# Kernel optimization log

Hardware: AMD Instinct MI355X
Metric: run time of the kernel (lower is better)

Reference implementation:

```python
import jax, jax.numpy as jnp
import numpy as np

E, B, L, H1, H2, C = 8, 4096, 512, 1024, 512, 40


def setup_inputs() -> dict:
    key = jax.random.key(0)
    ks = jax.random.split(key, 9)
    return {
        "x_s": jax.random.normal(ks[0], (B, L), jnp.float32),
        "x_p": jax.random.normal(ks[1], (B, L), jnp.float32),
        "W1": jax.random.normal(ks[2], (E, 2 * L, H1), jnp.float32) / np.sqrt(2 * L).astype(np.float32),
        "b1": jax.random.normal(ks[3], (E, H1), jnp.float32) * 0.01,
        "W2": jax.random.normal(ks[4], (E, H1, H2), jnp.float32) / np.sqrt(H1).astype(np.float32),
        "b2": jax.random.normal(ks[5], (E, H2), jnp.float32) * 0.01,
        "W3": jax.random.normal(ks[6], (E, H2, C), jnp.float32) / np.sqrt(H2).astype(np.float32),
        "b3": jax.random.normal(ks[7], (E, C), jnp.float32) * 0.01,
        "sub_module_label": jax.random.randint(ks[8], (B,), 0, E, dtype=jnp.int32),
        "sub_id": 0,
    }


def reference(x_s, x_p, W1, b1, W2, b2, W3, b3, sub_module_label, sub_id):
    # Encoders (EEGNet/SCN/DCN) abstracted as identity: x_s / x_p are latent features.
    # Cls_HEAD.forward: x = cat([x_p, x_s], dim=1); per-sample routed 3-layer ELU MLP head.
    # Dropout is identity in eval mode.
    x = jnp.concatenate([x_p, x_s], axis=1)                      # [B, 2L]
    h = jax.nn.elu(jnp.einsum('bi,eih->ebh', x, W1) + b1[:, None, :])   # [E, B, H1]
    h = jax.nn.elu(jnp.einsum('ebh,ehk->ebk', h, W2) + b2[:, None, :])  # [E, B, H2]
    out_all = jnp.einsum('ebk,ekc->ebc', h, W3) + b3[:, None, :]        # [E, B, C]
    # select each sample's routed expert output
    bidx = jnp.arange(x.shape[0])
    return out_all[sub_module_label, bidx]                       # [B, C]
```

## Files before the change

kernel.cpp:

```cpp
#include <hip/hip_runtime.h>
#include <hip/hip_bf16.h>
#include <math.h>

#define En   8
#define Bn   4096
#define Ln   512
#define K1n  1024
#define H1n  1024
#define H2n  512
#define Cn   40
#define NP3  48

typedef unsigned short u16;
typedef __attribute__((ext_vector_type(8))) short bf16x8;
typedef __attribute__((ext_vector_type(4))) float f32x4;

__device__ __forceinline__ u16 f2b(float f) {
    union { float f; unsigned int u; } v; v.f = f;
    unsigned int r = v.u + 0x7FFF + ((v.u >> 16) & 1);
    return (u16)(r >> 16);
}

__device__ __forceinline__ void g2l16(const void* g, void* l) {
    __builtin_amdgcn_global_load_lds(
        (const __attribute__((address_space(1))) unsigned int*)(unsigned long long)g,
        (__attribute__((address_space(3))) unsigned int*)(unsigned int)(unsigned long long)l,
        16, 0, 0);
}

#define PB_X0   1
#define PB_X    256
#define PB_W1   2048
#define PB_W2   1024
#define PB_W3   128
#define PB_TOT  (PB_X0 + PB_X + PB_W1 + PB_W2 + PB_W3)

__device__ __forceinline__ void wtrans64(
    const float* __restrict__ Wsrc, u16* __restrict__ Wdst,
    int K, int N, int k0, int n0, int tid, float* sm )
{
    #pragma unroll
    for (int s = 0; s < 4; s++) {
        int idx = tid + s * 256;
        int kk = idx >> 4, c4 = (idx & 15) * 4;
        float4 v = *(const float4*)&Wsrc[(size_t)(k0 + kk) * N + n0 + c4];
        float* row = sm + kk * 65 + c4;
        row[0] = v.x; row[1] = v.y; row[2] = v.z; row[3] = v.w;
    }
    __syncthreads();
    #pragma unroll
    for (int s = 0; s < 4; s++) {
        int idx = tid + s * 256;
        int nn = idx >> 4, kc = (idx & 15) * 4;
        ushort4 o = make_ushort4(f2b(sm[(kc + 0) * 65 + nn]), f2b(sm[(kc + 1) * 65 + nn]),
                                 f2b(sm[(kc + 2) * 65 + nn]), f2b(sm[(kc + 3) * 65 + nn]));
        *(ushort4*)&Wdst[(size_t)(n0 + nn) * K + k0 + kc] = o;
    }
}

__global__ __launch_bounds__(256) void prep_kernel(
    const float* __restrict__ xs, const float* __restrict__ xp,
    const float* __restrict__ W1, const float* __restrict__ W2,
    const float* __restrict__ W3, const int* __restrict__ label,
    int* __restrict__ meta, int* __restrict__ perm,
    u16* __restrict__ Xb, u16* __restrict__ W1t,
    u16* __restrict__ W2t, u16* __restrict__ W3t)
{
    __shared__ __align__(16) float sm[64 * 65];
    const int bid = blockIdx.x;
    const int tid = threadIdx.x;

    if (bid == 0) {
        int* cnt = (int*)sm;
        int* off = cnt + En;
        if (tid < En) cnt[tid] = 0;
        __syncthreads();
        for (int b = tid; b < Bn; b += 256) atomicAdd(&cnt[label[b]], 1);
        __syncthreads();
        if (tid == 0) {
            int run = 0;
            for (int e = 0; e < En; e++) { off[e] = run; run += cnt[e]; }
            off[En] = run;
        }
        __syncthreads();
        if (tid < En) cnt[tid] = off[tid];
        __syncthreads();
        for (int b = tid; b < Bn; b += 256) {
            int e = label[b];
            perm[atomicAdd(&cnt[e], 1)] = b;
        }
        if (tid <= En) meta[tid] = off[tid];
    } else if (bid < PB_X0 + PB_X) {
        int r0 = (bid - PB_X0) * 16;
        #pragma unroll 4
        for (int s = 0; s < 16; s++) {
            int r = r0 + s;
            int k = tid * 4;
            const float* src = (k < Ln) ? (xp + (size_t)r * Ln + k)
                                        : (xs + (size_t)r * Ln + (k - Ln));
            float4 v = *(const float4*)src;
            *(ushort4*)&Xb[(size_t)r * K1n + k] =
                make_ushort4(f2b(v.x), f2b(v.y), f2b(v.z), f2b(v.w));
        }
    } else if (bid < PB_X0 + PB_X + PB_W1) {
        int b = bid - (PB_X0 + PB_X);
        int e = b >> 8, rem = b & 255;
        int k0 = (rem >> 4) * 64, n0 = (rem & 15) * 64;
        wtrans64(W1 + (size_t)e * K1n * H1n, W1t + (size_t)e * H1n * K1n,
                 K1n, H1n, k0, n0, tid, sm);
    } else if (bid < PB_X0 + PB_X + PB_W1 + PB_W2) {
        int b = bid - (PB_X0 + PB_X + PB_W1);
        int e = b >> 7, rem = b & 127;
        int k0 = (rem >> 3) * 64, n0 = (rem & 7) * 64;
        wtrans64(W2 + (size_t)e * H1n * H2n, W2t + (size_t)e * H2n * H1n,
                 H1n, H2n, k0, n0, tid, sm);
    } else {
        int b = bid - (PB_X0 + PB_X + PB_W1 + PB_W2);
        int e = b >> 4, k0 = (b & 15) * 32;
        const float* src = W3 + (size_t)e * H2n * Cn;
        u16* dst = W3t + (size_t)e * NP3 * H2n;
        float* t = sm;
        #pragma unroll
        for (int s = 0; s < 5; s++) {
            int idx = tid + s * 256;
            int kk = idx / Cn, nn = idx - kk * Cn;
            if (kk < 32) t[kk * 41 + nn] = src[(size_t)(k0 + kk) * Cn + nn];
        }
        __syncthreads();
        #pragma unroll
        for (int s = 0; s < 6; s++) {
            int idx = tid + s * 256;
            int nn = idx >> 5, kk = idx & 31;
            float v = (nn < Cn) ? t[kk * 41 + nn] : 0.f;
            dst[(size_t)nn * H2n + k0 + kk] = f2b(v);
        }
    }
}

template <int K, int N, bool GATHER>
__global__ __launch_bounds__(256) void mfma_gemm(
    const u16* __restrict__ A, const u16* __restrict__ Wt,
    const float* __restrict__ bias, const int* __restrict__ meta,
    const int* __restrict__ perm, u16* __restrict__ out)
{
    constexpr int TM = 128, TN = 128, BK = 32;
    __shared__ __align__(16) u16 As[TM * BK];
    __shared__ __align__(16) u16 Bs[TN * BK];
    __shared__ int s_off[En + 1];

    const int tid = threadIdx.x;
    if (tid <= En) s_off[tid] = meta[tid];
    __syncthreads();

    int expert = -1, row0 = 0, acc_t = 0;
    const int bx = blockIdx.x;
    for (int e = 0; e < En; e++) {
        int c = s_off[e + 1] - s_off[e];
        int t = (c + TM - 1) / TM;
        if (expert < 0 && bx < acc_t + t) {
            expert = e;
            row0 = s_off[e] + (bx - acc_t) * TM;
        }
        acc_t += t;
    }
    if (expert < 0) return;
    const int rowmax = s_off[expert + 1] - 1;

    const int col0 = blockIdx.y * TN;
    const u16* Wexp = Wt + (size_t)expert * N * K;

    const int lane = tid & 63;
    const int wid = tid >> 6;
    const int wm = (wid & 1) * 64;
    const int wn = (wid >> 1) * 64;
    const int l15 = lane & 15;
    const int lq = lane >> 4;

    const u16* aptr[2];
    const u16* bptr[2];
    u16* alds[2]; u16* blds[2];
    #pragma unroll
    for (int s = 0; s < 2; s++) {
        int idx = tid + s * 256;
        int rl = idx >> 2, c = idx & 3;
        int kq = c ^ (rl & 3);
        int rg = row0 + rl; if (rg > rowmax) rg = rowmax;
        if (GATHER) rg = perm[rg];
        aptr[s] = A + (size_t)rg * K + kq * 8;
        bptr[s] = Wexp + (size_t)(col0 + rl) * K + kq * 8;
        alds[s] = &As[idx * 8];
        blds[s] = &Bs[idx * 8];
    }

    const int rsw = l15 & 3;

    f32x4 acc[4][4];
    #pragma unroll
    for (int i = 0; i < 4; i++)
        #pragma unroll
        for (int j = 0; j < 4; j++) acc[i][j] = (f32x4){0.f, 0.f, 0.f, 0.f};

    for (int k0 = 0; k0 < K; k0 += BK) {
        #pragma unroll
        for (int s = 0; s < 2; s++) {
            g2l16(aptr[s] + k0, alds[s]);
            g2l16(bptr[s] + k0, blds[s]);
        }
        __syncthreads();

        const int ksw = (lq ^ rsw) * 8;
        bf16x8 af[4], bf[4];
        #pragma unroll
        for (int i = 0; i < 4; i++)
            af[i] = *(const bf16x8*)&As[(wm + i * 16 + l15) * BK + ksw];
        #pragma unroll
        for (int j = 0; j < 4; j++)
            bf[j] = *(const bf16x8*)&Bs[(wn + j * 16 + l15) * BK + ksw];

        #pragma unroll
        for (int i = 0; i < 4; i++)
            #pragma unroll
            for (int j = 0; j < 4; j++)
                acc[i][j] = __builtin_amdgcn_mfma_f32_16x16x32_bf16(
                    af[i], bf[j], acc[i][j], 0, 0, 0);
        __syncthreads();
    }

    #pragma unroll
    for (int i = 0; i < 4; i++) {
        #pragma unroll
        for (int j = 0; j < 4; j++) {
            int col = col0 + wn + j * 16 + l15;
            float bv = bias[expert * N + col];
            #pragma unroll
            for (int r = 0; r < 4; r++) {
                int grow = row0 + wm + i * 16 + lq * 4 + r;
                if (grow <= rowmax) {
                    float v = acc[i][j][r] + bv;
                    v = (v > 0.f) ? v : (expf(v) - 1.f);
                    out[(size_t)grow * N + col] = f2b(v);
                }
            }
        }
    }
}

__global__ __launch_bounds__(256) void gemm3_mfma(
    const u16* __restrict__ h2, const u16* __restrict__ Wt3,
    const float* __restrict__ b3, const int* __restrict__ meta,
    const int* __restrict__ perm, float* __restrict__ out)
{
    constexpr int TM = 64, BK = 32;
    __shared__ __align__(16) u16 As[TM * BK];
    __shared__ __align__(16) u16 Bs[NP3 * BK];
    __shared__ int s_off[En + 1];

    const int tid = threadIdx.x;
    if (tid <= En) s_off[tid] = meta[tid];
    __syncthreads();

    int expert = -1, row0 = 0, acc_t = 0;
    const int bx = blockIdx.x;
    for (int e = 0; e < En; e++) {
        int c = s_off[e + 1] - s_off[e];
        int t = (c + TM - 1) / TM;
        if (expert < 0 && bx < acc_t + t) {
            expert = e;
            row0 = s_off[e] + (bx - acc_t) * TM;
        }
        acc_t += t;
    }
    if (expert < 0) return;
    const int rowmax = s_off[expert + 1] - 1;

    const int lane = tid & 63;
    const int wid = tid >> 6;
    const int l15 = lane & 15;
    const int lq = lane >> 4;

    const int rl = tid >> 2, c = tid & 3;
    const int kq = c ^ (rl & 3);
    int rg = row0 + rl; if (rg > rowmax) rg = rowmax;
    const u16* ag = h2 + (size_t)rg * H2n + kq * 8;
    const u16* bg = Wt3 + (size_t)expert * NP3 * H2n + (size_t)rl * H2n + kq * 8;
    u16* al = &As[tid * 8];
    u16* bl = &Bs[tid * 8];

    f32x4 acc[3];
    #pragma unroll
    for (int j = 0; j < 3; j++) acc[j] = (f32x4){0.f, 0.f, 0.f, 0.f};

    for (int k0 = 0; k0 < H2n; k0 += BK) {
        g2l16(ag + k0, al);
        if (tid < NP3 * 4) g2l16(bg + k0, bl);
        __syncthreads();

        const int ksw = (lq ^ (l15 & 3)) * 8;
        bf16x8 af = *(const bf16x8*)&As[(wid * 16 + l15) * BK + ksw];
        bf16x8 bf[3];
        #pragma unroll
        for (int j = 0; j < 3; j++)
            bf[j] = *(const bf16x8*)&Bs[(j * 16 + l15) * BK + ksw];
        #pragma unroll
        for (int j = 0; j < 3; j++)
            acc[j] = __builtin_amdgcn_mfma_f32_16x16x32_bf16(af, bf[j], acc[j], 0, 0, 0);
        __syncthreads();
    }

    #pragma unroll
    for (int j = 0; j < 3; j++) {
        int col = j * 16 + l15;
        if (col < Cn) {
            float bv = b3[expert * Cn + col];
            #pragma unroll
            for (int r = 0; r < 4; r++) {
                int grow = row0 + wid * 16 + lq * 4 + r;
                if (grow <= rowmax) {
                    int smp = perm[grow];
                    out[(size_t)smp * Cn + col] = acc[j][r] + bv;
                }
            }
        }
    }
}

extern "C" void kernel_launch(void* const* d_in, const int* in_sizes, int n_in,
                              void* d_out, int out_size, void* d_ws, size_t ws_size,
                              hipStream_t stream)
{
    const float* xs = (const float*)d_in[0];
    const float* xp = (const float*)d_in[1];
    const float* W1 = (const float*)d_in[2];
    const float* b1 = (const float*)d_in[3];
    const float* W2 = (const float*)d_in[4];
    const float* b2 = (const float*)d_in[5];
    const float* W3 = (const float*)d_in[6];
    const float* b3 = (const float*)d_in[7];
    const int* label = (const int*)d_in[8];
    float* out = (float*)d_out;

    char* ws = (char*)d_ws;
    int* meta = (int*)ws;
    int* perm = (int*)(ws + 64);
    u16* Xb  = (u16*)(ws + (64 << 10));
    u16* h2b = Xb;
    u16* W1t = (u16*)(ws + (64 << 10) + (8  << 20));
    u16* W2t = (u16*)(ws + (64 << 10) + (24 << 20));
    u16* h1b = (u16*)(ws + (64 << 10) + (32 << 20));
    u16* W3t = (u16*)(ws + (64 << 10) + (40 << 20));

    prep_kernel<<<PB_TOT, 256, 0, stream>>>(
        xs, xp, W1, W2, W3, label, meta, perm, Xb, W1t, W2t, W3t);

    mfma_gemm<K1n, H1n, true><<<dim3(40, H1n / 128), 256, 0, stream>>>(
        Xb, W1t, b1, meta, perm, h1b);
    mfma_gemm<H1n, H2n, false><<<dim3(40, H2n / 128), 256, 0, stream>>>(
        h1b, W2t, b2, meta, perm, h2b);

    gemm3_mfma<<<72, 256, 0, stream>>>(h2b, W3t, b3, meta, perm, out);
}
```

Measured before the change: 192.8 us.

## Fuse layer-3 GEMM into layer-2 epilogue and double-buffer GEMM K-loop

The third GEMM is folded into the layer-2 kernel epilogue. Each block stages its ELU'd h2 tile in LDS, multiplies it by the matching 128-column slice of W3, and atomically adds partial logits into the output, which the prep kernel pre-initialises with the per-sample b3 bias. The main GEMM loop also moves to BK=64 with double-buffered LDS prefetch and an 8-way XOR swizzle, to overlap global loads with MFMA work. This removes one launch and the h2 round-trip through memory, at the cost of float atomics (ordering changes rounding) and more LDS per block.

```diff
diff --git a/kernel.cpp b/kernel.cpp
--- a/kernel.cpp
+++ b/kernel.cpp
@@ -33,7 +33,8 @@
 #define PB_W1   2048
 #define PB_W2   1024
 #define PB_W3   128
-#define PB_TOT  (PB_X0 + PB_X + PB_W1 + PB_W2 + PB_W3)
+#define PB_OUT  64
+#define PB_TOT  (PB_X0 + PB_X + PB_W1 + PB_W2 + PB_W3 + PB_OUT)
 
 __device__ __forceinline__ void wtrans64(
     const float* __restrict__ Wsrc, u16* __restrict__ Wdst,
@@ -61,10 +62,12 @@
 __global__ __launch_bounds__(256) void prep_kernel(
     const float* __restrict__ xs, const float* __restrict__ xp,
     const float* __restrict__ W1, const float* __restrict__ W2,
-    const float* __restrict__ W3, const int* __restrict__ label,
+    const float* __restrict__ W3, const float* __restrict__ b3,
+    const int* __restrict__ label,
     int* __restrict__ meta, int* __restrict__ perm,
     u16* __restrict__ Xb, u16* __restrict__ W1t,
-    u16* __restrict__ W2t, u16* __restrict__ W3t)
+    u16* __restrict__ W2t, u16* __restrict__ W3t,
+    float* __restrict__ out)
 {
     __shared__ __align__(16) float sm[64 * 65];
     const int bid = blockIdx.x;
@@ -114,7 +117,7 @@
         int k0 = (rem >> 3) * 64, n0 = (rem & 7) * 64;
         wtrans64(W2 + (size_t)e * H1n * H2n, W2t + (size_t)e * H2n * H1n,
                  H1n, H2n, k0, n0, tid, sm);
-    } else {
+    } else if (bid < PB_X0 + PB_X + PB_W1 + PB_W2 + PB_W3) {
         int b = bid - (PB_X0 + PB_X + PB_W1 + PB_W2);
         int e = b >> 4, k0 = (b & 15) * 32;
         const float* src = W3 + (size_t)e * H2n * Cn;
@@ -134,37 +137,46 @@
             float v = (nn < Cn) ? t[kk * 41 + nn] : 0.f;
             dst[(size_t)nn * H2n + k0 + kk] = f2b(v);
         }
-    }
-}
-
-template <int K, int N, bool GATHER>
+    } else {
+        int b = bid - (PB_X0 + PB_X + PB_W1 + PB_W2 + PB_W3);
+        int r0 = b * 64;
+        #pragma unroll
+        for (int s = 0; s < 10; s++) {
+            int idx = tid + s * 256;
+            int r = r0 + idx / Cn;
+            int c = idx - (idx / Cn) * Cn;
+            out[(size_t)r * Cn + c] = b3[label[r] * Cn + c];
+        }
+    }
+}
+
+template <int K, int N, bool GATHER, bool FUSE3>
 __global__ __launch_bounds__(256) void mfma_gemm(
     const u16* __restrict__ A, const u16* __restrict__ Wt,
     const float* __restrict__ bias, const int* __restrict__ meta,
-    const int* __restrict__ perm, u16* __restrict__ out)
+    const int* __restrict__ perm, u16* __restrict__ outb,
+    const u16* __restrict__ Wt3, float* __restrict__ outf)
 {
-    constexpr int TM = 128, TN = 128, BK = 32;
-    __shared__ __align__(16) u16 As[TM * BK];
-    __shared__ __align__(16) u16 Bs[TN * BK];
-    __shared__ int s_off[En + 1];
+    constexpr int TM = 128, TN = 128, BK = 64;
+    constexpr int T = K / BK;
+    __shared__ __align__(16) u16 SM[32768];
 
     const int tid = threadIdx.x;
-    if (tid <= En) s_off[tid] = meta[tid];
-    __syncthreads();
-
-    int expert = -1, row0 = 0, acc_t = 0;
     const int bx = blockIdx.x;
+
+    int expert = -1, row0 = 0, rowmax = 0, acc_t = 0;
+    int prev = meta[0];
+    #pragma unroll
     for (int e = 0; e < En; e++) {
-        int c = s_off[e + 1] - s_off[e];
+        int nxt = meta[e + 1];
+        int c = nxt - prev;
         int t = (c + TM - 1) / TM;
         if (expert < 0 && bx < acc_t + t) {
-            expert = e;
-            row0 = s_off[e] + (bx - acc_t) * TM;
-        }
-        acc_t += t;
+            expert = e; row0 = prev + (bx - acc_t) * TM; rowmax = nxt - 1;
+        }
+        acc_t += t; prev = nxt;
     }
     if (expert < 0) return;
-    const int rowmax = s_off[expert + 1] - 1;
 
     const int col0 = blockIdx.y * TN;
     const u16* Wexp = Wt + (size_t)expert * N * K;
@@ -176,23 +188,21 @@
     const int l15 = lane & 15;
     const int lq = lane >> 4;
 
-    const u16* aptr[2];
-    const u16* bptr[2];
-    u16* alds[2]; u16* blds[2];
-    #pragma unroll
-    for (int s = 0; s < 2; s++) {
+    const u16* aptr[4]; const u16* bptr[4];
+    int aoff[4], boff[4];
+    #pragma unroll
+    for (int s = 0; s < 4; s++) {
         int idx = tid + s * 256;
-        int rl = idx >> 2, c = idx & 3;
-        int kq = c ^ (rl & 3);
+        int rl = idx >> 3, c = idx & 7;
+        int kq = c ^ (rl & 7);
         int rg = row0 + rl; if (rg > rowmax) rg = rowmax;
         if (GATHER) rg = perm[rg];
         aptr[s] = A + (size_t)rg * K + kq * 8;
         bptr[s] = Wexp + (size_t)(col0 + rl) * K + kq * 8;
-        alds[s] = &As[idx * 8];
-        blds[s] = &Bs[idx * 8];
-    }
-
-    const int rsw = l15 & 3;
+        aoff[s] = idx * 8;
+        boff[s] = 8192 + idx * 8;
+    }
+    const int csw = l15 & 7;
 
     f32x4 acc[4][4];
     #pragma unroll
@@ -200,124 +210,118 @@
         #pragma unroll
         for (int j = 0; j < 4; j++) acc[i][j] = (f32x4){0.f, 0.f, 0.f, 0.f};
 
-    for (int k0 = 0; k0 < K; k0 += BK) {
-        #pragma unroll
-        for (int s = 0; s < 2; s++) {
-            g2l16(aptr[s] + k0, alds[s]);
-            g2l16(bptr[s] + k0, blds[s]);
-        }
-        __syncthreads();
-
-        const int ksw = (lq ^ rsw) * 8;
-        bf16x8 af[4], bf[4];
-        #pragma unroll
-        for (int i = 0; i < 4; i++)
-            af[i] = *(const bf16x8*)&As[(wm + i * 16 + l15) * BK + ksw];
-        #pragma unroll
-        for (int j = 0; j < 4; j++)
-            bf[j] = *(const bf16x8*)&Bs[(wn + j * 16 + l15) * BK + ksw];
-
-        #pragma unroll
-        for (int i = 0; i < 4; i++)
+    #pragma unroll
+    for (int s = 0; s < 4; s++) {
+        g2l16(aptr[s], &SM[aoff[s]]);
+        g2l16(bptr[s], &SM[boff[s]]);
+    }
+
+    for (int t = 0; t < T; t++) {
+        __syncthreads();
+        const u16* As = &SM[(t & 1) * 16384];
+        const u16* Bs = As + 8192;
+        if (t + 1 < T) {
+            int base = ((t + 1) & 1) * 16384;
+            int ko = (t + 1) * BK;
+            #pragma unroll
+            for (int s = 0; s < 4; s++) {
+                g2l16(aptr[s] + ko, &SM[base + aoff[s]]);
+                g2l16(bptr[s] + ko, &SM[base + boff[s]]);
+            }
+        }
+        bf16x8 af[4][2], bf[4][2];
+        #pragma unroll
+        for (int h = 0; h < 2; h++) {
+            const int ksw = (((h * 4 + lq) ^ csw)) * 8;
+            #pragma unroll
+            for (int i = 0; i < 4; i++)
+                af[i][h] = *(const bf16x8*)&As[(wm + i * 16 + l15) * BK + ksw];
             #pragma unroll
             for (int j = 0; j < 4; j++)
-                acc[i][j] = __builtin_amdgcn_mfma_f32_16x16x32_bf16(
-                    af[i], bf[j], acc[i][j], 0, 0, 0);
-        __syncthreads();
-    }
-
-    #pragma unroll
-    for (int i = 0; i < 4; i++) {
-        #pragma unroll
-        for (int j = 0; j < 4; j++) {
-            int col = col0 + wn + j * 16 + l15;
-            float bv = bias[expert * N + col];
-            #pragma unroll
-            for (int r = 0; r < 4; r++) {
-                int grow = row0 + wm + i * 16 + lq * 4 + r;
-                if (grow <= rowmax) {
+                bf[j][h] = *(const bf16x8*)&Bs[(wn + j * 16 + l15) * BK + ksw];
+        }
+        #pragma unroll
+        for (int h = 0; h < 2; h++)
+            #pragma unroll
+            for (int i = 0; i < 4; i++)
+                #pragma unroll
+                for (int j = 0; j < 4; j++)
+                    acc[i][j] = __builtin_amdgcn_mfma_f32_16x16x32_bf16(
+                        af[i][h], bf[j][h], acc[i][j], 0, 0, 0);
+    }
+
+    if (!FUSE3) {
+        #pragma unroll
+        for (int i = 0; i < 4; i++) {
+            #pragma unroll
+            for (int j = 0; j < 4; j++) {
+                int col = col0 + wn + j * 16 + l15;
+                float bv = bias[expert * N + col];
+                #pragma unroll
+                for (int r = 0; r < 4; r++) {
+                    int grow = row0 + wm + i * 16 + lq * 4 + r;
+                    if (grow <= rowmax) {
+                        float v = acc[i][j][r] + bv;
+                        v = (v > 0.f) ? v : (expf(v) - 1.f);
+                        outb[(size_t)grow * N + col] = f2b(v);
+                    }
+                }
+            }
+        }
+    } else {
+        __syncthreads();
+        u16* H = &SM[0];
+        #pragma unroll
+        for (int i = 0; i < 4; i++) {
+            #pragma unroll
+            for (int j = 0; j < 4; j++) {
+                int col = wn + j * 16 + l15;
+                float bv = bias[expert * N + col0 + col];
+                #pragma unroll
+                for (int r = 0; r < 4; r++) {
                     float v = acc[i][j][r] + bv;
                     v = (v > 0.f) ? v : (expf(v) - 1.f);
-                    out[(size_t)grow * N + col] = f2b(v);
+                    H[(wm + i * 16 + lq * 4 + r) * 136 + col] = f2b(v);
                 }
             }
         }
-    }
-}
-
-__global__ __launch_bounds__(256) void gemm3_mfma(
-    const u16* __restrict__ h2, const u16* __restrict__ Wt3,
-    const float* __restrict__ b3, const int* __restrict__ meta,
-    const int* __restrict__ perm, float* __restrict__ out)
-{
-    constexpr int TM = 64, BK = 32;
-    __shared__ __align__(16) u16 As[TM * BK];
-    __shared__ __align__(16) u16 Bs[NP3 * BK];
-    __shared__ int s_off[En + 1];
-
-    const int tid = threadIdx.x;
-    if (tid <= En) s_off[tid] = meta[tid];
-    __syncthreads();
-
-    int expert = -1, row0 = 0, acc_t = 0;
-    const int bx = blockIdx.x;
-    for (int e = 0; e < En; e++) {
-        int c = s_off[e + 1] - s_off[e];
-        int t = (c + TM - 1) / TM;
-        if (expert < 0 && bx < acc_t + t) {
-            expert = e;
-            row0 = s_off[e] + (bx - acc_t) * TM;
-        }
-        acc_t += t;
-    }
-    if (expert < 0) return;
-    const int rowmax = s_off[expert + 1] - 1;
-
-    const int lane = tid & 63;
-    const int wid = tid >> 6;
-    const int l15 = lane & 15;
-    const int lq = lane >> 4;
-
-    const int rl = tid >> 2, c = tid & 3;
-    const int kq = c ^ (rl & 3);
-    int rg = row0 + rl; if (rg > rowmax) rg = rowmax;
-    const u16* ag = h2 + (size_t)rg * H2n + kq * 8;
-    const u16* bg = Wt3 + (size_t)expert * NP3 * H2n + (size_t)rl * H2n + kq * 8;
-    u16* al = &As[tid * 8];
-    u16* bl = &Bs[tid * 8];
-
-    f32x4 acc[3];
-    #pragma unroll
-    for (int j = 0; j < 3; j++) acc[j] = (f32x4){0.f, 0.f, 0.f, 0.f};
-
-    for (int k0 = 0; k0 < H2n; k0 += BK) {
-        g2l16(ag + k0, al);
-        if (tid < NP3 * 4) g2l16(bg + k0, bl);
-        __syncthreads();
-
-        const int ksw = (lq ^ (l15 & 3)) * 8;
-        bf16x8 af = *(const bf16x8*)&As[(wid * 16 + l15) * BK + ksw];
-        bf16x8 bf[3];
-        #pragma unroll
-        for (int j = 0; j < 3; j++)
-            bf[j] = *(const bf16x8*)&Bs[(j * 16 + l15) * BK + ksw];
-        #pragma unroll
-        for (int j = 0; j < 3; j++)
-            acc[j] = __builtin_amdgcn_mfma_f32_16x16x32_bf16(af, bf[j], acc[j], 0, 0, 0);
-        __syncthreads();
-    }
-
-    #pragma unroll
-    for (int j = 0; j < 3; j++) {
-        int col = j * 16 + l15;
-        if (col < Cn) {
-            float bv = b3[expert * Cn + col];
-            #pragma unroll
-            for (int r = 0; r < 4; r++) {
-                int grow = row0 + wid * 16 + lq * 4 + r;
-                if (grow <= rowmax) {
-                    int smp = perm[grow];
-                    out[(size_t)smp * Cn + col] = acc[j][r] + bv;
+        __syncthreads();
+        const int rh = (wid & 1) * 64;
+        const int kb = (wid >> 1) * 64;
+        f32x4 a3[4][3];
+        #pragma unroll
+        for (int i = 0; i < 4; i++)
+            #pragma unroll
+            for (int j = 0; j < 3; j++) a3[i][j] = (f32x4){0.f, 0.f, 0.f, 0.f};
+        #pragma unroll
+        for (int ki = 0; ki < 2; ki++) {
+            int kl = kb + ki * 32;
+            bf16x8 ha[4];
+            #pragma unroll
+            for (int i = 0; i < 4; i++)
+                ha[i] = *(const bf16x8*)&H[(rh + i * 16 + l15) * 136 + kl + lq * 8];
+            #pragma unroll
+            for (int j = 0; j < 3; j++) {
+                bf16x8 wb = *(const bf16x8*)
+                    &Wt3[((size_t)expert * NP3 + j * 16 + l15) * H2n + col0 + kl + lq * 8];
+                #pragma unroll
+                for (int i = 0; i < 4; i++)
+                    a3[i][j] = __builtin_amdgcn_mfma_f32_16x16x32_bf16(
+                        ha[i], wb, a3[i][j], 0, 0, 0);
+            }
+        }
+        #pragma unroll
+        for (int j = 0; j < 3; j++) {
+            int col = j * 16 + l15;
+            if (col < Cn) {
+                #pragma unroll
+                for (int i = 0; i < 4; i++) {
+                    #pragma unroll
+                    for (int r = 0; r < 4; r++) {
+                        int grow = row0 + rh + i * 16 + lq * 4 + r;
+                        if (grow <= rowmax)
+                            atomicAdd(&outf[(size_t)perm[grow] * Cn + col], a3[i][j][r]);
+                    }
                 }
             }
         }
@@ -343,19 +347,17 @@
     int* meta = (int*)ws;
     int* perm = (int*)(ws + 64);
     u16* Xb  = (u16*)(ws + (64 << 10));
-    u16* h2b = Xb;
     u16* W1t = (u16*)(ws + (64 << 10) + (8  << 20));
     u16* W2t = (u16*)(ws + (64 << 10) + (24 << 20));
     u16* h1b = (u16*)(ws + (64 << 10) + (32 << 20));
     u16* W3t = (u16*)(ws + (64 << 10) + (40 << 20));
 
     prep_kernel<<<PB_TOT, 256, 0, stream>>>(
-        xs, xp, W1, W2, W3, label, meta, perm, Xb, W1t, W2t, W3t);
-
-    mfma_gemm<K1n, H1n, true><<<dim3(40, H1n / 128), 256, 0, stream>>>(
-        Xb, W1t, b1, meta, perm, h1b);
-    mfma_gemm<H1n, H2n, false><<<dim3(40, H2n / 128), 256, 0, stream>>>(
-        h1b, W2t, b2, meta, perm, h2b);
-
-    gemm3_mfma<<<72, 256, 0, stream>>>(h2b, W3t, b3, meta, perm, out);
-}
+        xs, xp, W1, W2, W3, b3, label, meta, perm, Xb, W1t, W2t, W3t, out);
+
+    mfma_gemm<K1n, H1n, true, false><<<dim3(40, 8), 256, 0, stream>>>(
+        Xb, W1t, b1, meta, perm, h1b, nullptr, nullptr);
+
+    mfma_gemm<H1n, H2n, false, true><<<dim3(40, 4), 256, 0, stream>>>(
+        h1b, W2t, b2, meta, perm, nullptr, W3t, out);
+}
```

After: 180.9 us. 6.2% less time.
